# Optimization experiments

Hardware: AMD Instinct MI355X
Metric: run time of the kernel (lower is better)

Reference implementation:

```python
import jax, jax.numpy as jnp
import numpy as np

B, S, E, H, SIG = 1, 2048, 1024, 16, 256
D = E // H // 2  # 32, differential head_dim
DEPTH = 1
LAMBDA_INIT = 0.8 - 0.6 * float(np.exp(-0.3 * DEPTH))


def _rope(x):
    # x: (b, s, heads, D); lucidrains RotaryEmbedding(dim=D//2, interleaved),
    # rotates first D//2 features, passes rest through. freqs_for='lang'.
    rot = D // 2
    inv = 1.0 / (10000.0 ** (jnp.arange(0, rot, 2, dtype=jnp.float32) / rot))
    t = jnp.arange(x.shape[1], dtype=jnp.float32)
    freqs = t[:, None] * inv[None, :]          # (s, rot//2)
    freqs = jnp.repeat(freqs, 2, axis=-1)      # (s, rot) interleaved
    cos = jnp.cos(freqs)[None, :, None, :]
    sin = jnp.sin(freqs)[None, :, None, :]
    xr, xp = x[..., :rot], x[..., rot:]
    x1, x2 = xr[..., 0::2], xr[..., 1::2]
    half = jnp.stack([-x2, x1], axis=-1).reshape(xr.shape)
    return jnp.concatenate([xr * cos + half * sin, xp], axis=-1)


def _rmsnorm(x, w, b, eps=1e-8):
    ms = jnp.mean(x * x, axis=-1, keepdims=True)
    return x * jax.lax.rsqrt(ms + eps) * w + b


def _layernorm(x, w, b, eps=1e-5):
    mu = jnp.mean(x, axis=-1, keepdims=True)
    var = jnp.mean((x - mu) ** 2, axis=-1, keepdims=True)
    return (x - mu) * jax.lax.rsqrt(var + eps) * w + b


def _causal_softmax(q, k, scale):
    # q,k: (b, s, h, d) -> probs (b, h, s, s)
    scores = jnp.einsum('bqhd,bkhd->bhqk', q, k) * scale
    mask = jnp.tril(jnp.ones((q.shape[1], q.shape[1]), dtype=bool))
    scores = jnp.where(mask[None, None], scores, jnp.finfo(scores.dtype).min)
    return jax.nn.softmax(scores, axis=-1)


def setup_inputs() -> dict:
    key = jax.random.key(0)
    ks = jax.random.split(key, 16)
    n = lambda k, shape, s=0.02: jax.random.normal(k, shape, dtype=jnp.float32) * s
    return {
        'x': jax.random.normal(ks[0], (B, S, E), dtype=jnp.float32),
        'emb': jax.random.normal(ks[1], (B, SIG), dtype=jnp.float32),
        'qkv_w': n(ks[2], (3 * E, E)),
        'out_w': n(ks[3], (E, E)),
        'sigma_w': n(ks[4], (D, SIG)),
        'lq1': n(ks[5], (D,), 0.1), 'lk1': n(ks[6], (D,), 0.1),
        'lq2': n(ks[7], (D,), 0.1), 'lk2': n(ks[8], (D,), 0.1),
        'ln_w': jnp.ones((2 * D,), jnp.float32), 'ln_b': jnp.zeros((2 * D,), jnp.float32),
        'ln1_w': jnp.ones((E,), jnp.float32), 'ln1_b': jnp.zeros((E,), jnp.float32),
        'ln2_w': jnp.ones((E,), jnp.float32), 'ln2_b': jnp.zeros((E,), jnp.float32),
        'w1': n(ks[9], (4 * E, E)), 'b1': jnp.zeros((4 * E,), jnp.float32),
        'w2': n(ks[10], (E, 4 * E)), 'b2': jnp.zeros((E,), jnp.float32),
    }


def reference(x, emb, qkv_w, out_w, sigma_w, lq1, lk1, lq2, lk2,
              ln_w, ln_b, ln1_w, ln1_b, ln2_w, ln2_b, w1, b1, w2, b2):
    b, s, e = x.shape
    sig = emb @ sigma_w.T                              # (b, D)
    qkv = x @ qkv_w.T                                  # (b, s, 3e)
    q, k, v = jnp.split(qkv, 3, axis=-1)
    q = _rope(q.reshape(b, s, 2 * H, D)).reshape(b, s, H, 2, D)
    k = _rope(k.reshape(b, s, 2 * H, D)).reshape(b, s, H, 2, D)
    v = v.reshape(b, s, H, 2, D)
    q1, q2 = q[..., 0, :], q[..., 1, :]
    k1, k2 = k[..., 0, :], k[..., 1, :]
    v1, v2 = v[..., 0, :], v[..., 1, :]
    sb = sig[:, None, None, :]
    q2 = q2 + sb
    k2 = k2 + sb
    scale = D ** -0.5
    p1 = _causal_softmax(q1, k1, scale)                # shared softmax for v1/v2
    a11 = jnp.einsum('bhqk,bkhd->bqhd', p1, v1)
    a12 = jnp.einsum('bhqk,bkhd->bqhd', p1, v2)
    attn1 = jnp.concatenate([a11, a12], axis=-1)       # (b, s, H, 2D)
    p2 = _causal_softmax(q2, k2, scale)
    a21 = jnp.einsum('bhqk,bkhd->bqhd', p2, v1)
    a22 = jnp.einsum('bhqk,bkhd->bqhd', p2, v2)
    attn2 = jnp.concatenate([a21, a22], axis=-1)
    lam = jnp.exp(jnp.sum(lq1 * lk1)) - jnp.exp(jnp.sum(lq2 * lk2)) + LAMBDA_INIT
    a = _rmsnorm(attn1 - lam * attn2, ln_w, ln_b) * (1.0 - LAMBDA_INIT)
    a = a.reshape(b, s, e) @ out_w.T
    h = _layernorm(a + x, ln1_w, ln1_b)
    ff = jax.nn.silu(h @ w1.T + b1) @ w2.T + b2        # dropout off (eval)
    return _layernorm(ff + h, ln2_w, ln2_b)
```

## Files before the change

### kernel.cpp

```cpp
#include <hip/hip_runtime.h>
#include <hip/hip_bf16.h>
#include <math.h>


#define S_LEN 2048
#define E_DIM 1024
#define H_NUM 16
#define D_DIM 32
#define SIG_DIM 256

#define LAMBDA_INIT 0.3555090675909693f
#define ONE_MINUS_LAMBDA_INIT 0.6444909324090307f

typedef __bf16 v8bf __attribute__((ext_vector_type(8)));
typedef __bf16 v4bf __attribute__((ext_vector_type(4)));
typedef float f32x4 __attribute__((ext_vector_type(4)));
static_assert(sizeof(v8bf) == 16, "v8bf must be 16B");

#define B_QKV   0
#define B_G     8388608
#define B_XB    25165824
#define B_ATTN  25165824
#define B_T1    25165824
#define B_HB    33554432
#define B_T2    33554432
#define B_ANRM  41943040
#define B_HBUF  41943040
#define B_QWB   50331648
#define B_OWB   0
#define B_W1B   0
#define B_W2B   0
#define B_TAB   56623104

__global__ __launch_bounds__(256) void tab_kernel(float* __restrict__ tab) {
    int t = blockIdx.x * 256 + threadIdx.x;
    int s = t >> 3;
    int pi = t & 7;
    double inv = pow(10000.0, -(double)pi / 8.0);
    double ph = (double)s * inv;
    tab[t]         = (float)cos(ph);
    tab[16384 + t] = (float)sin(ph);
}

__global__ __launch_bounds__(64) void sig_lam_kernel(
    const float* __restrict__ emb, const float* __restrict__ sigma_w,
    const float* __restrict__ lq1, const float* __restrict__ lk1,
    const float* __restrict__ lq2, const float* __restrict__ lk2,
    float* __restrict__ sig, float* __restrict__ lam)
{
    int t = threadIdx.x;
    if (t < 32) {
        float acc = 0.f;
        for (int j = 0; j < SIG_DIM; ++j)
            acc = fmaf(emb[j], sigma_w[t * SIG_DIM + j], acc);
        sig[t] = acc;
    } else if (t == 32) {
        float s1 = 0.f, s2 = 0.f;
        for (int d = 0; d < D_DIM; ++d) {
            s1 = fmaf(lq1[d], lk1[d], s1);
            s2 = fmaf(lq2[d], lk2[d], s2);
        }
        lam[0] = expf(s1) - expf(s2) + LAMBDA_INIT;
    }
}

__global__ __launch_bounds__(256) void f2b_kernel(
    const float* __restrict__ in, __bf16* __restrict__ out, int n)
{
    int base = (blockIdx.x * 256 + threadIdx.x) * 8;
    if (base >= n) return;
    float4 v0 = *(const float4*)(in + base);
    float4 v1 = *(const float4*)(in + base + 4);
    v8bf o;
    o[0] = (__bf16)v0.x; o[1] = (__bf16)v0.y; o[2] = (__bf16)v0.z; o[3] = (__bf16)v0.w;
    o[4] = (__bf16)v1.x; o[5] = (__bf16)v1.y; o[6] = (__bf16)v1.z; o[7] = (__bf16)v1.w;
    *(v8bf*)(out + base) = o;
}

__device__ __forceinline__ void gload_lds16(const __bf16* g, __bf16* l) {
    __builtin_amdgcn_global_load_lds(
        (const __attribute__((address_space(1))) unsigned int*)g,
        (__attribute__((address_space(3))) unsigned int*)l, 16, 0, 0);
}

template<bool BIAS, bool SILU, bool RES, bool OBF16>
__global__ __launch_bounds__(256) void mgemm_kernel(
    const __bf16* __restrict__ A, const __bf16* __restrict__ B,
    float* __restrict__ C, __bf16* __restrict__ Cb,
    int M, int N, int K,
    const float* __restrict__ bias, const float* __restrict__ res)
{
    __shared__ __bf16 As[128][32];
    __shared__ __bf16 Bs[128][32];

    const int tid  = threadIdx.x;
    const int wid  = tid >> 6;
    const int lane = tid & 63;
    const int m0 = blockIdx.y * 128;
    const int n0 = blockIdx.x * 128;
    const int wr = (wid >> 1) * 64;
    const int wc = (wid & 1) * 64;
    const int lrow = lane & 15;
    const int kg   = lane >> 4;

    f32x4 acc[4][4];
#pragma unroll
    for (int mi = 0; mi < 4; ++mi)
#pragma unroll
        for (int ni = 0; ni < 4; ++ni) acc[mi][ni] = (f32x4){0.f, 0.f, 0.f, 0.f};

    const int srow = lane >> 2;
    const int sfi  = lane & 3;
    const __bf16* Ap0 = A + (size_t)(m0 + wid * 16 + srow) * K + sfi * 8;
    const __bf16* Ap1 = Ap0 + (size_t)64 * K;
    const __bf16* Bp0 = B + (size_t)(n0 + wid * 16 + srow) * K + sfi * 8;
    const __bf16* Bp1 = Bp0 + (size_t)64 * K;
    __bf16* Al0 = &As[wid * 16][0];
    __bf16* Al1 = &As[64 + wid * 16][0];
    __bf16* Bl0 = &Bs[wid * 16][0];
    __bf16* Bl1 = &Bs[64 + wid * 16][0];

    for (int k0 = 0; k0 < K; k0 += 32) {
        __syncthreads();
        gload_lds16(Ap0 + k0, Al0);
        gload_lds16(Ap1 + k0, Al1);
        gload_lds16(Bp0 + k0, Bl0);
        gload_lds16(Bp1 + k0, Bl1);
        __syncthreads();

        v8bf a[4], b[4];
#pragma unroll
        for (int mi = 0; mi < 4; ++mi)
            a[mi] = *(const v8bf*)&As[wr + mi * 16 + lrow][kg * 8];
#pragma unroll
        for (int ni = 0; ni < 4; ++ni)
            b[ni] = *(const v8bf*)&Bs[wc + ni * 16 + lrow][kg * 8];
#pragma unroll
        for (int mi = 0; mi < 4; ++mi)
#pragma unroll
            for (int ni = 0; ni < 4; ++ni)
                acc[mi][ni] = __builtin_amdgcn_mfma_f32_16x16x32_bf16(
                    a[mi], b[ni], acc[mi][ni], 0, 0, 0);
    }

    const int crow = (lane >> 4) * 4;
    const int ccol = lane & 15;
#pragma unroll
    for (int mi = 0; mi < 4; ++mi) {
#pragma unroll
        for (int ni = 0; ni < 4; ++ni) {
            const int col = n0 + wc + ni * 16 + ccol;
            float bv = 0.f;
            if (BIAS) bv = bias[col];
#pragma unroll
            for (int j = 0; j < 4; ++j) {
                const int row = m0 + wr + mi * 16 + crow + j;
                float v = acc[mi][ni][j] + bv;
                if (SILU) v = v / (1.f + expf(-v));
                if (RES) v += res[(size_t)row * N + col];
                if (OBF16) Cb[(size_t)row * N + col] = (__bf16)v;
                else       C[(size_t)row * N + col] = v;
            }
        }
    }
}

__global__ __launch_bounds__(256) void rope_kernel(
    float* __restrict__ qkv, const float* __restrict__ tab,
    const float* __restrict__ sig)
{
    int t = blockIdx.x * 256 + threadIdx.x;
    int s    = t >> 6;
    int sub  = t & 63;
    int part = sub >> 5;
    int rh   = sub & 31;
    float* p = qkv + (size_t)s * 3072 + part * E_DIM + rh * D_DIM;
    const float* ct = tab + s * 8;
    const float* st = tab + 16384 + s * 8;

    float v[16];
#pragma unroll
    for (int i = 0; i < 4; ++i) *(float4*)(v + i * 4) = *(const float4*)(p + i * 4);
    float o[16];
#pragma unroll
    for (int pi = 0; pi < 8; ++pi) {
        float c = ct[pi], sn = st[pi];
        float x1 = v[2 * pi], x2 = v[2 * pi + 1];
        o[2 * pi]     = x1 * c - x2 * sn;
        o[2 * pi + 1] = x2 * c + x1 * sn;
    }
    if (rh & 1) {
#pragma unroll
        for (int i = 0; i < 16; ++i) o[i] += sig[i];
        float u[16];
#pragma unroll
        for (int i = 0; i < 4; ++i) *(float4*)(u + i * 4) = *(const float4*)(p + 16 + i * 4);
#pragma unroll
        for (int i = 0; i < 16; ++i) u[i] += sig[16 + i];
#pragma unroll
        for (int i = 0; i < 4; ++i) *(float4*)(p + 16 + i * 4) = *(const float4*)(u + i * 4);
    }
#pragma unroll
    for (int i = 0; i < 4; ++i) *(float4*)(p + i * 4) = *(const float4*)(o + i * 4);
}

__global__ __launch_bounds__(256, 2) void fattn_kernel(
    const float* __restrict__ qkv, float* __restrict__ attn)
{
    __shared__ __bf16 Ks[2048];
    __shared__ __bf16 Vt[4096];
    __shared__ __bf16 Pl[4096];

    const int bid = blockIdx.x;
    const int rb = bid & 31;
    const int ah = bid >> 5;
    const int h = ah >> 1;
    const int a = ah & 1;
    const int rh = 2 * h + a;
    const int i0 = rb * 64;
    const int tid = threadIdx.x;
    const int wq = tid >> 6;
    const int lane = tid & 63;
    const int c = lane & 15;
    const int g = lane >> 4;

    const float scale = 0.17677669529663687f;
    const float* qp = qkv + (size_t)(i0 + wq * 16 + c) * 3072 + rh * 32 + g * 8;
    float4 q0 = *(const float4*)qp;
    float4 q1 = *(const float4*)(qp + 4);
    v8bf qf;
    qf[0] = (__bf16)(q0.x * scale); qf[1] = (__bf16)(q0.y * scale);
    qf[2] = (__bf16)(q0.z * scale); qf[3] = (__bf16)(q0.w * scale);
    qf[4] = (__bf16)(q1.x * scale); qf[5] = (__bf16)(q1.y * scale);
    qf[6] = (__bf16)(q1.z * scale); qf[7] = (__bf16)(q1.w * scale);

    f32x4 o_acc[4];
#pragma unroll
    for (int nj = 0; nj < 4; ++nj) o_acc[nj] = (f32x4){0.f, 0.f, 0.f, 0.f};
    float m_run[4] = {-3.0e38f, -3.0e38f, -3.0e38f, -3.0e38f};
    float l_run[4] = {0.f, 0.f, 0.f, 0.f};

    const int sk_key = tid >> 2, sk_ds = tid & 3;
    const int sk_slot = (((sk_key * 4 + sk_ds) ^ ((sk_key >> 1) & 3)) * 8);
    const int sv_k = tid >> 2, sv_dg = tid & 3;
    const int pbase = wq * 1024;

    for (int jt = 0; jt <= rb; ++jt) {
        const int j0 = jt * 64;
        __syncthreads();
        {
            const float* src = qkv + (size_t)(j0 + sk_key) * 3072 + E_DIM + rh * 32 + sk_ds * 8;
            float4 a0 = *(const float4*)src;
            float4 a1 = *(const float4*)(src + 4);
            v8bf kb;
            kb[0] = (__bf16)a0.x; kb[1] = (__bf16)a0.y; kb[2] = (__bf16)a0.z; kb[3] = (__bf16)a0.w;
            kb[4] = (__bf16)a1.x; kb[5] = (__bf16)a1.y; kb[6] = (__bf16)a1.z; kb[7] = (__bf16)a1.w;
            *(v8bf*)&Ks[sk_slot] = kb;
        }
        {
            const float* src = qkv + (size_t)(j0 + sv_k) * 3072 + 2 * E_DIM + h * 64 + sv_dg * 16;
            float4 v0 = *(const float4*)src;
            float4 v1 = *(const float4*)(src + 4);
            float4 v2 = *(const float4*)(src + 8);
            float4 v3 = *(const float4*)(src + 12);
            float vv[16] = {v0.x, v0.y, v0.z, v0.w, v1.x, v1.y, v1.z, v1.w,
                            v2.x, v2.y, v2.z, v2.w, v3.x, v3.y, v3.z, v3.w};
#pragma unroll
            for (int e = 0; e < 16; ++e) {
                int d = sv_dg * 16 + e;
                Vt[(d * 64 + sv_k) ^ ((d & 7) << 3)] = (__bf16)vv[e];
            }
        }
        __syncthreads();

        f32x4 s[4];
#pragma unroll
        for (int ni = 0; ni < 4; ++ni) {
            int slot = ((((16 * ni + c) * 4 + g) ^ ((c >> 1) & 3)) * 8);
            v8bf kf = *(const v8bf*)&Ks[slot];
            s[ni] = __builtin_amdgcn_mfma_f32_16x16x32_bf16(
                qf, kf, (f32x4){0.f, 0.f, 0.f, 0.f}, 0, 0, 0);
        }
        if (jt == rb) {
#pragma unroll
            for (int ni = 0; ni < 4; ++ni)
#pragma unroll
                for (int r = 0; r < 4; ++r)
                    if (16 * ni + c > wq * 16 + 4 * g + r) s[ni][r] = -3.0e38f;
        }

        float p[4][4];
#pragma unroll
        for (int r = 0; r < 4; ++r) {
            float t = fmaxf(fmaxf(s[0][r], s[1][r]), fmaxf(s[2][r], s[3][r]));
            t = fmaxf(t, __shfl_xor(t, 1, 64));
            t = fmaxf(t, __shfl_xor(t, 2, 64));
            t = fmaxf(t, __shfl_xor(t, 4, 64));
            t = fmaxf(t, __shfl_xor(t, 8, 64));
            float mnew = fmaxf(m_run[r], t);
            float corr = __expf(m_run[r] - mnew);
            m_run[r] = mnew;
            l_run[r] *= corr;
#pragma unroll
            for (int nj = 0; nj < 4; ++nj) o_acc[nj][r] *= corr;
#pragma unroll
            for (int ni = 0; ni < 4; ++ni) {
                float pp = __expf(s[ni][r] - mnew);
                p[ni][r] = pp;
                l_run[r] += pp;
            }
        }

#pragma unroll
        for (int ni = 0; ni < 4; ++ni)
#pragma unroll
            for (int r = 0; r < 4; ++r) {
                int q = 4 * g + r;
                Pl[pbase + ((q * 64 + 16 * ni + c) ^ ((q & 7) << 3))] = (__bf16)p[ni][r];
            }
        asm volatile("s_waitcnt lgkmcnt(0)" ::: "memory");
        __builtin_amdgcn_sched_barrier(0);

        v8bf pa[2];
#pragma unroll
        for (int kj = 0; kj < 2; ++kj)
            pa[kj] = *(const v8bf*)&Pl[pbase + ((c * 64 + kj * 32 + g * 8) ^ ((c & 7) << 3))];
#pragma unroll
        for (int nj = 0; nj < 4; ++nj) {
            int d = 16 * nj + c;
#pragma unroll
            for (int kj = 0; kj < 2; ++kj) {
                v8bf vb = *(const v8bf*)&Vt[(d * 64 + kj * 32 + g * 8) ^ ((c & 7) << 3)];
                o_acc[nj] = __builtin_amdgcn_mfma_f32_16x16x32_bf16(
                    pa[kj], vb, o_acc[nj], 0, 0, 0);
            }
        }
    }

#pragma unroll
    for (int r = 0; r < 4; ++r) {
        float lt = l_run[r];
        lt += __shfl_xor(lt, 1, 64);
        lt += __shfl_xor(lt, 2, 64);
        lt += __shfl_xor(lt, 4, 64);
        lt += __shfl_xor(lt, 8, 64);
        l_run[r] = 1.0f / lt;
    }
#pragma unroll
    for (int nj = 0; nj < 4; ++nj)
#pragma unroll
        for (int r = 0; r < 4; ++r) {
            int qg = i0 + wq * 16 + 4 * g + r;
            attn[((size_t)a * S_LEN + qg) * E_DIM + h * 64 + 16 * nj + c] =
                o_acc[nj][r] * l_run[r];
        }
}

__global__ __launch_bounds__(256) void diffnorm_kernel(
    const float* __restrict__ attn, const float* __restrict__ ln_w,
    const float* __restrict__ ln_b, const float* __restrict__ lamp,
    __bf16* __restrict__ out)
{
    int g = blockIdx.x * 4 + (threadIdx.x >> 6);
    int lane = threadIdx.x & 63;
    int s = g >> 4;
    int h = g & 15;
    float lam = lamp[0];
    const float* p1 = attn + (size_t)s * E_DIM + h * 64;
    const float* p2 = attn + (size_t)(S_LEN + s) * E_DIM + h * 64;
    float c = p1[lane] - lam * p2[lane];
    float sq = c * c;
#pragma unroll
    for (int off = 32; off >= 1; off >>= 1) sq += __shfl_xor(sq, off, 64);
    float ms = sq * (1.0f / 64.0f);
    float r = 1.0f / sqrtf(ms + 1e-8f);
    float o = (c * r * ln_w[lane] + ln_b[lane]) * ONE_MINUS_LAMBDA_INIT;
    out[(size_t)s * E_DIM + h * 64 + lane] = (__bf16)o;
}

__global__ __launch_bounds__(256) void ln_kernel(
    const float* __restrict__ in, const float* __restrict__ w,
    const float* __restrict__ b, float* __restrict__ out,
    __bf16* __restrict__ outb)
{
    __shared__ float red[4];
    int row = blockIdx.x;
    int t = threadIdx.x;
    const float* xr = in + (size_t)row * E_DIM + t * 4;
    float4 v = *(const float4*)xr;
    float s = v.x + v.y + v.z + v.w;
#pragma unroll
    for (int off = 32; off >= 1; off >>= 1) s += __shfl_xor(s, off, 64);
    if ((t & 63) == 0) red[t >> 6] = s;
    __syncthreads();
    float mu = (red[0] + red[1] + red[2] + red[3]) * (1.0f / 1024.0f);
    __syncthreads();
    float dx0 = v.x - mu, dx1 = v.y - mu, dx2 = v.z - mu, dx3 = v.w - mu;
    float sq = dx0 * dx0 + dx1 * dx1 + dx2 * dx2 + dx3 * dx3;
#pragma unroll
    for (int off = 32; off >= 1; off >>= 1) sq += __shfl_xor(sq, off, 64);
    if ((t & 63) == 0) red[t >> 6] = sq;
    __syncthreads();
    float var = (red[0] + red[1] + red[2] + red[3]) * (1.0f / 1024.0f);
    float r = 1.0f / sqrtf(var + 1e-5f);
    float4 wv = *(const float4*)(w + t * 4);
    float4 bv = *(const float4*)(b + t * 4);
    float4 o;
    o.x = dx0 * r * wv.x + bv.x;
    o.y = dx1 * r * wv.y + bv.y;
    o.z = dx2 * r * wv.z + bv.z;
    o.w = dx3 * r * wv.w + bv.w;
    *(float4*)(out + (size_t)row * E_DIM + t * 4) = o;
    if (outb) {
        v4bf ob;
        ob[0] = (__bf16)o.x; ob[1] = (__bf16)o.y;
        ob[2] = (__bf16)o.z; ob[3] = (__bf16)o.w;
        *(v4bf*)(outb + (size_t)row * E_DIM + t * 4) = ob;
    }
}

extern "C" void kernel_launch(void* const* d_in, const int* in_sizes, int n_in,
                              void* d_out, int out_size, void* d_ws, size_t ws_size,
                              hipStream_t stream)
{
    const float* x       = (const float*)d_in[0];
    const float* emb     = (const float*)d_in[1];
    const float* qkv_w   = (const float*)d_in[2];
    const float* out_w   = (const float*)d_in[3];
    const float* sigma_w = (const float*)d_in[4];
    const float* lq1     = (const float*)d_in[5];
    const float* lk1     = (const float*)d_in[6];
    const float* lq2     = (const float*)d_in[7];
    const float* lk2     = (const float*)d_in[8];
    const float* ln_w    = (const float*)d_in[9];
    const float* ln_b    = (const float*)d_in[10];
    const float* ln1_w   = (const float*)d_in[11];
    const float* ln1_b   = (const float*)d_in[12];
    const float* ln2_w   = (const float*)d_in[13];
    const float* ln2_b   = (const float*)d_in[14];
    const float* w1      = (const float*)d_in[15];
    const float* b1      = (const float*)d_in[16];
    const float* w2      = (const float*)d_in[17];
    const float* b2      = (const float*)d_in[18];
    float* out = (float*)d_out;
    char* ws = (char*)d_ws;

    float*  qkv  = (float*)(ws + B_QKV);
    __bf16* g    = (__bf16*)(ws + B_G);
    __bf16* xb   = (__bf16*)(ws + B_XB);
    float*  attn = (float*)(ws + B_ATTN);
    float*  t1   = (float*)(ws + B_T1);
    __bf16* hb   = (__bf16*)(ws + B_HB);
    float*  t2   = (float*)(ws + B_T2);
    __bf16* anrm = (__bf16*)(ws + B_ANRM);
    float*  hbuf = (float*)(ws + B_HBUF);
    __bf16* qwb  = (__bf16*)(ws + B_QWB);
    __bf16* owb  = (__bf16*)(ws + B_OWB);
    __bf16* w1b  = (__bf16*)(ws + B_W1B);
    __bf16* w2b  = (__bf16*)(ws + B_W2B);
    float*  tab  = (float*)(ws + B_TAB);
    float*  sig  = tab + 32768;
    float*  lam  = tab + 32800;

    tab_kernel<<<64, 256, 0, stream>>>(tab);
    sig_lam_kernel<<<1, 64, 0, stream>>>(emb, sigma_w, lq1, lk1, lq2, lk2, sig, lam);
    f2b_kernel<<<1024, 256, 0, stream>>>(x, xb, 2097152);
    f2b_kernel<<<1536, 256, 0, stream>>>(qkv_w, qwb, 3145728);
    mgemm_kernel<false, false, false, false><<<dim3(24, 16), 256, 0, stream>>>(
        xb, qwb, qkv, (__bf16*)0, 2048, 3072, 1024, (const float*)0, (const float*)0);
    rope_kernel<<<512, 256, 0, stream>>>(qkv, tab, sig);
    fattn_kernel<<<1024, 256, 0, stream>>>(qkv, attn);
    diffnorm_kernel<<<8192, 256, 0, stream>>>(attn, ln_w, ln_b, lam, anrm);
    f2b_kernel<<<512, 256, 0, stream>>>(out_w, owb, 1048576);
    mgemm_kernel<false, false, true, false><<<dim3(8, 16), 256, 0, stream>>>(
        anrm, owb, t1, (__bf16*)0, 2048, 1024, 1024, (const float*)0, x);
    ln_kernel<<<2048, 256, 0, stream>>>(t1, ln1_w, ln1_b, hbuf, hb);
    f2b_kernel<<<2048, 256, 0, stream>>>(w1, w1b, 4194304);
    mgemm_kernel<true, true, false, true><<<dim3(32, 16), 256, 0, stream>>>(
        hb, w1b, (float*)0, g, 2048, 4096, 1024, b1, (const float*)0);
    f2b_kernel<<<2048, 256, 0, stream>>>(w2, w2b, 4194304);
    mgemm_kernel<true, false, true, false><<<dim3(8, 16), 256, 0, stream>>>(
        g, w2b, t2, (__bf16*)0, 2048, 1024, 4096, b2, hbuf);
    ln_kernel<<<2048, 256, 0, stream>>>(t2, ln2_w, ln2_b, out, (__bf16*)0);
}
```

Before: 478.1 us.

## Double-buffer K/V tiles in attention and balance causal block scheduling

```diff
diff --git a/kernel.cpp b/kernel.cpp
--- a/kernel.cpp
+++ b/kernel.cpp
@@ -207,13 +207,15 @@
 __global__ __launch_bounds__(256, 2) void fattn_kernel(
     const float* __restrict__ qkv, float* __restrict__ attn)
 {
-    __shared__ __bf16 Ks[2048];
-    __shared__ __bf16 Vt[4096];
+    __shared__ __bf16 Ks[2][2048];
+    __shared__ __bf16 Vt[2][4096];
     __shared__ __bf16 Pl[4096];
 
-    const int bid = blockIdx.x;
-    const int rb = bid & 31;
-    const int ah = bid >> 5;
+    const int phys = blockIdx.x;
+    const int virt = (phys & 7) * 128 + (phys >> 3);
+    const int ah = virt >> 5;
+    const int u  = virt & 31;
+    const int rb = (u & 1) ? (u >> 1) : (31 - (u >> 1));
     const int h = ah >> 1;
     const int a = ah & 1;
     const int rh = 2 * h + a;
@@ -244,40 +246,49 @@
     const int sk_slot = (((sk_key * 4 + sk_ds) ^ ((sk_key >> 1) & 3)) * 8);
     const int sv_k = tid >> 2, sv_dg = tid & 3;
     const int pbase = wq * 1024;
+    const float* kbase = qkv + E_DIM + rh * 32 + sk_ds * 8;
+    const float* vbase = qkv + 2 * E_DIM + h * 64 + sv_dg * 16;
+
+    {
+        const float* ksrc = kbase + (size_t)sk_key * 3072;
+        float4 pk0 = *(const float4*)ksrc;
+        float4 pk1 = *(const float4*)(ksrc + 4);
+        const float* vsrc = vbase + (size_t)sv_k * 3072;
+        float4 pv0 = *(const float4*)vsrc;
+        float4 pv1 = *(const float4*)(vsrc + 4);
+        float4 pv2 = *(const float4*)(vsrc + 8);
+        float4 pv3 = *(const float4*)(vsrc + 12);
+        v8bf kb;
+        kb[0] = (__bf16)pk0.x; kb[1] = (__bf16)pk0.y; kb[2] = (__bf16)pk0.z; kb[3] = (__bf16)pk0.w;
+        kb[4] = (__bf16)pk1.x; kb[5] = (__bf16)pk1.y; kb[6] = (__bf16)pk1.z; kb[7] = (__bf16)pk1.w;
+        *(v8bf*)&Ks[0][sk_slot] = kb;
+        float vv[16] = {pv0.x, pv0.y, pv0.z, pv0.w, pv1.x, pv1.y, pv1.z, pv1.w,
+                        pv2.x, pv2.y, pv2.z, pv2.w, pv3.x, pv3.y, pv3.z, pv3.w};
+#pragma unroll
+        for (int e = 0; e < 16; ++e) {
+            int d = sv_dg * 16 + e;
+            Vt[0][(d * 64 + sv_k) ^ ((d & 7) << 3)] = (__bf16)vv[e];
+        }
+    }
+    __syncthreads();
 
     for (int jt = 0; jt <= rb; ++jt) {
-        const int j0 = jt * 64;
-        __syncthreads();
-        {
-            const float* src = qkv + (size_t)(j0 + sk_key) * 3072 + E_DIM + rh * 32 + sk_ds * 8;
-            float4 a0 = *(const float4*)src;
-            float4 a1 = *(const float4*)(src + 4);
-            v8bf kb;
-            kb[0] = (__bf16)a0.x; kb[1] = (__bf16)a0.y; kb[2] = (__bf16)a0.z; kb[3] = (__bf16)a0.w;
-            kb[4] = (__bf16)a1.x; kb[5] = (__bf16)a1.y; kb[6] = (__bf16)a1.z; kb[7] = (__bf16)a1.w;
-            *(v8bf*)&Ks[sk_slot] = kb;
-        }
-        {
-            const float* src = qkv + (size_t)(j0 + sv_k) * 3072 + 2 * E_DIM + h * 64 + sv_dg * 16;
-            float4 v0 = *(const float4*)src;
-            float4 v1 = *(const float4*)(src + 4);
-            float4 v2 = *(const float4*)(src + 8);
-            float4 v3 = *(const float4*)(src + 12);
-            float vv[16] = {v0.x, v0.y, v0.z, v0.w, v1.x, v1.y, v1.z, v1.w,
-                            v2.x, v2.y, v2.z, v2.w, v3.x, v3.y, v3.z, v3.w};
-#pragma unroll
-            for (int e = 0; e < 16; ++e) {
-                int d = sv_dg * 16 + e;
-                Vt[(d * 64 + sv_k) ^ ((d & 7) << 3)] = (__bf16)vv[e];
-            }
-        }
-        __syncthreads();
+        const int cur = jt & 1;
+        const int jn = (jt < rb) ? (jt + 1) * 64 : 0;
+        const float* ksrc = kbase + (size_t)(jn + sk_key) * 3072;
+        float4 pk0 = *(const float4*)ksrc;
+        float4 pk1 = *(const float4*)(ksrc + 4);
+        const float* vsrc = vbase + (size_t)(jn + sv_k) * 3072;
+        float4 pv0 = *(const float4*)vsrc;
+        float4 pv1 = *(const float4*)(vsrc + 4);
+        float4 pv2 = *(const float4*)(vsrc + 8);
+        float4 pv3 = *(const float4*)(vsrc + 12);
 
         f32x4 s[4];
 #pragma unroll
         for (int ni = 0; ni < 4; ++ni) {
             int slot = ((((16 * ni + c) * 4 + g) ^ ((c >> 1) & 3)) * 8);
-            v8bf kf = *(const v8bf*)&Ks[slot];
+            v8bf kf = *(const v8bf*)&Ks[cur][slot];
             s[ni] = __builtin_amdgcn_mfma_f32_16x16x32_bf16(
                 qf, kf, (f32x4){0.f, 0.f, 0.f, 0.f}, 0, 0, 0);
         }
@@ -330,11 +341,26 @@
             int d = 16 * nj + c;
 #pragma unroll
             for (int kj = 0; kj < 2; ++kj) {
-                v8bf vb = *(const v8bf*)&Vt[(d * 64 + kj * 32 + g * 8) ^ ((c & 7) << 3)];
+                v8bf vb = *(const v8bf*)&Vt[cur][(d * 64 + kj * 32 + g * 8) ^ ((c & 7) << 3)];
                 o_acc[nj] = __builtin_amdgcn_mfma_f32_16x16x32_bf16(
                     pa[kj], vb, o_acc[nj], 0, 0, 0);
             }
         }
+
+        {
+            v8bf kb;
+            kb[0] = (__bf16)pk0.x; kb[1] = (__bf16)pk0.y; kb[2] = (__bf16)pk0.z; kb[3] = (__bf16)pk0.w;
+            kb[4] = (__bf16)pk1.x; kb[5] = (__bf16)pk1.y; kb[6] = (__bf16)pk1.z; kb[7] = (__bf16)pk1.w;
+            *(v8bf*)&Ks[cur ^ 1][sk_slot] = kb;
+            float vv[16] = {pv0.x, pv0.y, pv0.z, pv0.w, pv1.x, pv1.y, pv1.z, pv1.w,
+                            pv2.x, pv2.y, pv2.z, pv2.w, pv3.x, pv3.y, pv3.z, pv3.w};
+#pragma unroll
+            for (int e = 0; e < 16; ++e) {
+                int d = sv_dg * 16 + e;
+                Vt[cur ^ 1][(d * 64 + sv_k) ^ ((d & 7) << 3)] = (__bf16)vv[e];
+            }
+        }
+        __syncthreads();
     }
 
 #pragma unroll
```

Result: faster. 438.1 us (-8.4%).
